# Kernel optimization log

Measured on AMD Instinct MI355X. Metric: run time of the kernel, lower is better.

## Reference

```python
import jax, jax.numpy as jnp
import numpy as np

N_NODES = 50000


def gcn_conv(x, row, col, deg_inv_sqrt, W, b, num_nodes):
    # PyG GCNConv: h = x @ W; out[i] = sum_{(j->i)} norm_ji * h[j] + b
    # norm_ji = deg^{-1/2}[j] * deg^{-1/2}[i], with self-loops already in (row, col).
    h = x @ W  # [N, C_out]
    norm = deg_inv_sqrt[row] * deg_inv_sqrt[col]  # [E+N]
    msgs = h[row] * norm[:, None]  # gather + scale, [E+N, C_out]
    out = jax.ops.segment_sum(msgs, col, num_segments=num_nodes)
    return out + b


def setup_inputs() -> dict:
    key = jax.random.key(0)
    ks = jax.random.split(key, 8)
    n, e = N_NODES, 1600000
    c_in, c_hid, c_out = 128, 64, 32
    x = jax.random.normal(ks[0], (n, c_in), dtype=jnp.float32)
    edge_index = jax.random.randint(ks[1], (2, e), 0, n, dtype=jnp.int64)
    s1 = 1.0 / np.sqrt(c_in)
    s2 = 1.0 / np.sqrt(c_hid)
    W1 = jax.random.uniform(ks[2], (c_in, c_hid), jnp.float32, -s1, s1)
    b1 = jnp.zeros((c_hid,), jnp.float32)
    W2 = jax.random.uniform(ks[3], (c_hid, c_out), jnp.float32, -s2, s2)
    b2 = jnp.zeros((c_out,), jnp.float32)
    W3 = jax.random.uniform(ks[4], (c_hid, c_out), jnp.float32, -s2, s2)
    b3 = jnp.zeros((c_out,), jnp.float32)
    return {"x": x, "edge_index": edge_index, "W1": W1, "b1": b1,
            "W2": W2, "b2": b2, "W3": W3, "b3": b3}


def reference(x, edge_index, W1, b1, W2, b2, W3, b3):
    n = x.shape[0]
    # add self-loops (PyG GCNConv default add_self_loops=True)
    loop = jnp.arange(n, dtype=edge_index.dtype)
    row = jnp.concatenate([edge_index[0], loop])
    col = jnp.concatenate([edge_index[1], loop])
    # symmetric normalization: deg computed over target nodes (unit edge weights)
    deg = jax.ops.segment_sum(jnp.ones_like(col, dtype=x.dtype), col, num_segments=n)
    deg_inv_sqrt = jnp.where(deg > 0, jax.lax.rsqrt(jnp.maximum(deg, 1.0)), 0.0)
    h = jax.nn.relu(gcn_conv(x, row, col, deg_inv_sqrt, W1, b1, n))
    mu = gcn_conv(h, row, col, deg_inv_sqrt, W2, b2, n)
    logvar = gcn_conv(h, row, col, deg_inv_sqrt, W3, b3, n)
    return (mu, logvar)
```

## Files before the change

### kernel.cpp

```cpp
#include <hip/hip_runtime.h>


#define NBMAX 256
#define NT2 256
#define SLOT 128
#define CAPSH 14
#define CAP (1 << CAPSH)

typedef unsigned int uint4v __attribute__((ext_vector_type(4)));
typedef float float4v __attribute__((ext_vector_type(4)));

__device__ __forceinline__ ushort f2bf(float x) {
    unsigned u = __float_as_uint(x);
    u = (u + 0x7FFFu + ((u >> 16) & 1u)) >> 16;
    return (ushort)u;
}
__device__ __forceinline__ float bflo(unsigned u) { return __uint_as_float(u << 16); }
__device__ __forceinline__ float bfhi(unsigned u) { return __uint_as_float(u & 0xFFFF0000u); }

__device__ __forceinline__ void acc8(float* a, uint4 x) {
    a[0] += bflo(x.x); a[1] += bfhi(x.x);
    a[2] += bflo(x.y); a[3] += bfhi(x.y);
    a[4] += bflo(x.z); a[5] += bfhi(x.z);
    a[6] += bflo(x.w); a[7] += bfhi(x.w);
}

__device__ __forceinline__ unsigned sc2(unsigned u, float d) {
    return (unsigned)f2bf(d * bflo(u)) | ((unsigned)f2bf(d * bfhi(u)) << 16);
}

__global__ __launch_bounds__(256) void k_front(const int* __restrict__ row,
                                               const int* __restrict__ col,
                                               const float* __restrict__ x,
                                               const float* __restrict__ W1,
                                               int* __restrict__ binbuf,
                                               unsigned char* __restrict__ cnt,
                                               ushort* __restrict__ hs1b,
                                               int n, int e, int chunk) {
    __shared__ __align__(16) unsigned char smem[16384];
    int t = threadIdx.x;
    if (blockIdx.x < NT2) {
        int* lh = (int*)smem;
        int tile = blockIdx.x;
        int t0 = tile * chunk;
        int t1 = t0 + chunk < e ? t0 + chunk : e;
        for (int i = t; i < NBMAX; i += 256) lh[i] = 0;
        __syncthreads();
        for (int i = t0 + t; i < t1; i += 256) {
            int c = col[i];
            int b = c >> 8;
            int pos = atomicAdd(&lh[b], 1);
            if (pos < SLOT)
                binbuf[(((b << 8) + tile) << 7) + pos] = row[i] | ((c & 255) << 16);
        }
        __syncthreads();
        for (int b = t; b < NBMAX; b += 256) {
            int c = lh[b];
            cnt[(tile << 8) + b] = (unsigned char)(c < SLOT ? c : SLOT);
        }
    } else {
        float4 (*ws)[64] = reinterpret_cast<float4(*)[64]>(smem);
        float4 (*xs)[16][8] = reinterpret_cast<float4(*)[16][8]>(smem + 8192);
        int wid = t >> 6;
        int lane = t & 63;
        int r0 = (blockIdx.x - NT2) * 64 + wid * 16;
        const float4* x4 = (const float4*)x;
        const float4* W4g = (const float4*)W1;
        float acc[16];
#pragma unroll
        for (int r = 0; r < 16; ++r) acc[r] = 0.f;
#pragma unroll
        for (int st = 0; st < 4; ++st) {
            if (st) __syncthreads();
#pragma unroll
            for (int j = 0; j < 2; ++j) {
                int f = j * 256 + t;
                float4 wv = W4g[st * 512 + f];
                int klocal = f >> 4;
                int c0 = (f & 15) * 4;
                int k4 = klocal >> 2, comp = klocal & 3;
                ((float*)&ws[k4][c0])[comp]     = wv.x;
                ((float*)&ws[k4][c0 + 1])[comp] = wv.y;
                ((float*)&ws[k4][c0 + 2])[comp] = wv.z;
                ((float*)&ws[k4][c0 + 3])[comp] = wv.w;
            }
#pragma unroll
            for (int j = 0; j < 2; ++j) {
                int idx = j * 64 + lane;
                int rr = r0 + (idx >> 3);
                if (rr >= n) rr = n - 1;
                xs[wid][idx >> 3][idx & 7] = x4[(size_t)rr * 32 + st * 8 + (idx & 7)];
            }
            __syncthreads();
#pragma unroll 2
            for (int k4 = 0; k4 < 8; ++k4) {
                float4 wv = ws[k4][lane];
#pragma unroll
                for (int r = 0; r < 16; ++r) {
                    float4 xv = xs[wid][r][k4];
                    acc[r] = fmaf(xv.x, wv.x, acc[r]);
                    acc[r] = fmaf(xv.y, wv.y, acc[r]);
                    acc[r] = fmaf(xv.z, wv.z, acc[r]);
                    acc[r] = fmaf(xv.w, wv.w, acc[r]);
                }
            }
        }
        ushort* hb = hs1b + (size_t)(lane >> 5) * n * 32 + (lane & 31);
#pragma unroll
        for (int r = 0; r < 16; ++r) {
            int rw = r0 + r;
            if (rw < n) hb[(size_t)rw * 32] = f2bf(acc[r]);
        }
    }
}

__global__ __launch_bounds__(256) void k_build(const int* __restrict__ binbuf,
                                               const unsigned char* __restrict__ cnt,
                                               float* __restrict__ dis,
                                               int* __restrict__ rp2,
                                               ushort* __restrict__ csr,
                                               ushort* __restrict__ hs1b, int n) {
    __shared__ int lcnt[256], s[256], cur[256];
    __shared__ float sdis[256];
    int b = blockIdx.x;
    int t = threadIdx.x;
    int myc = cnt[(t << 8) + b];
    int mybase = ((b << 8) + t) << 7;
    lcnt[t] = 0;
    __syncthreads();
    for (int i = 0; i < myc; ++i) {
        int p = binbuf[mybase + i];
        atomicAdd(&lcnt[(p >> 16) & 255], 1);
    }
    __syncthreads();
    int v = lcnt[t];
    s[t] = v;
    __syncthreads();
    for (int off = 1; off < 256; off <<= 1) {
        int u = (t >= off) ? s[t - off] : 0;
        __syncthreads();
        s[t] += u;
        __syncthreads();
    }
    int node0 = b << 8;
    int nloc = n - node0 < 256 ? n - node0 : 256;
    int lo = b << CAPSH;
    if (t < nloc) {
        int beg = lo + s[t] - v;
        rp2[2 * (node0 + t)] = beg;
        rp2[2 * (node0 + t) + 1] = beg + v;
        cur[t] = beg;
        float dv = rsqrtf((float)v + 1.0f);
        dis[node0 + t] = dv;
        sdis[t] = dv;
    }
    __syncthreads();
    for (int i = 0; i < myc; ++i) {
        int p = binbuf[mybase + i];
        int pos = atomicAdd(&cur[(p >> 16) & 255], 1);
        csr[pos] = (ushort)(p & 0xffff);
    }
    uint4* s0 = (uint4*)hs1b + (size_t)node0 * 4;
    uint4* s1 = (uint4*)hs1b + (size_t)n * 4 + (size_t)node0 * 4;
    for (int idx = t; idx < nloc * 4; idx += 256) {
        float dv = sdis[idx >> 2];
        uint4 u0 = s0[idx], u1 = s1[idx];
        u0.x = sc2(u0.x, dv); u0.y = sc2(u0.y, dv);
        u0.z = sc2(u0.z, dv); u0.w = sc2(u0.w, dv);
        u1.x = sc2(u1.x, dv); u1.y = sc2(u1.y, dv);
        u1.z = sc2(u1.z, dv); u1.w = sc2(u1.w, dv);
        s0[idx] = u0;
        s1[idx] = u1;
    }
}

__global__ __launch_bounds__(256) void k_pull1(const int* __restrict__ rp2,
                                               const ushort* __restrict__ csr,
                                               const ushort* __restrict__ hs1b,
                                               const float* __restrict__ dis,
                                               const float* __restrict__ b1,
                                               ushort* __restrict__ hs2b, int n) {
    int xcd = blockIdx.x & 7;
    int sid = xcd >> 2;
    int idx = (blockIdx.x >> 3) * 4 + (xcd & 3);
    int node = idx * 64 + (threadIdx.x >> 2);
    int c4 = threadIdx.x & 3;
    if (node >= n) return;
    size_t slab = (size_t)sid * n * 32;
    const uint4* h4 = (const uint4*)(hs1b + slab);
    int2 be = ((const int2*)rp2)[node];
    float a[8], b[8];
    uint4 v = h4[(size_t)node * 4 + c4];
    a[0] = bflo(v.x); a[1] = bfhi(v.x); a[2] = bflo(v.y); a[3] = bfhi(v.y);
    a[4] = bflo(v.z); a[5] = bfhi(v.z); a[6] = bflo(v.w); a[7] = bfhi(v.w);
#pragma unroll
    for (int j = 0; j < 8; ++j) b[j] = 0.f;
    int k = be.x;
    for (; k + 8 <= be.y; k += 8) {
        uint4 v0 = h4[(size_t)csr[k] * 4 + c4];
        uint4 v1 = h4[(size_t)csr[k + 1] * 4 + c4];
        uint4 v2 = h4[(size_t)csr[k + 2] * 4 + c4];
        uint4 v3 = h4[(size_t)csr[k + 3] * 4 + c4];
        uint4 v4 = h4[(size_t)csr[k + 4] * 4 + c4];
        uint4 v5 = h4[(size_t)csr[k + 5] * 4 + c4];
        uint4 v6 = h4[(size_t)csr[k + 6] * 4 + c4];
        uint4 v7 = h4[(size_t)csr[k + 7] * 4 + c4];
        acc8(a, v0); acc8(b, v1); acc8(a, v2); acc8(b, v3);
        acc8(a, v4); acc8(b, v5); acc8(a, v6); acc8(b, v7);
    }
    if (k + 4 <= be.y) {
        uint4 v0 = h4[(size_t)csr[k] * 4 + c4];
        uint4 v1 = h4[(size_t)csr[k + 1] * 4 + c4];
        uint4 v2 = h4[(size_t)csr[k + 2] * 4 + c4];
        uint4 v3 = h4[(size_t)csr[k + 3] * 4 + c4];
        acc8(a, v0); acc8(b, v1); acc8(a, v2); acc8(b, v3);
        k += 4;
    }
    for (; k < be.y; ++k) acc8(a, h4[(size_t)csr[k] * 4 + c4]);
    float d = dis[node];
    const float* b1s = b1 + sid * 32;
    float4 bb0 = *(const float4*)(b1s + c4 * 8);
    float4 bb1 = *(const float4*)(b1s + c4 * 8 + 4);
    float bj[8] = {bb0.x, bb0.y, bb0.z, bb0.w, bb1.x, bb1.y, bb1.z, bb1.w};
    float o[8];
#pragma unroll
    for (int j = 0; j < 8; ++j) {
        float tt = fmaf(d, a[j] + b[j], bj[j]);
        o[j] = tt > 0.f ? d * tt : 0.f;
    }
    uint4v w;
    w.x = (unsigned)f2bf(o[0]) | ((unsigned)f2bf(o[1]) << 16);
    w.y = (unsigned)f2bf(o[2]) | ((unsigned)f2bf(o[3]) << 16);
    w.z = (unsigned)f2bf(o[4]) | ((unsigned)f2bf(o[5]) << 16);
    w.w = (unsigned)f2bf(o[6]) | ((unsigned)f2bf(o[7]) << 16);
    __builtin_nontemporal_store(w, (uint4v*)((uint4*)(hs2b + slab) + (size_t)node * 4 + c4));
}

__global__ __launch_bounds__(256) void k_pull2(const int* __restrict__ rp2,
                                               const ushort* __restrict__ csr,
                                               const ushort* __restrict__ hs2b,
                                               const float* __restrict__ dis,
                                               float* __restrict__ gagg, int n) {
    int xcd = blockIdx.x & 7;
    int sid = xcd >> 2;
    int idx = (blockIdx.x >> 3) * 4 + (xcd & 3);
    int node = idx * 64 + (threadIdx.x >> 2);
    int c4 = threadIdx.x & 3;
    if (node >= n) return;
    const uint4* h4 = (const uint4*)(hs2b + (size_t)sid * n * 32);
    int2 be = ((const int2*)rp2)[node];
    float a[8], b[8];
    uint4 v = h4[(size_t)node * 4 + c4];
    a[0] = bflo(v.x); a[1] = bfhi(v.x); a[2] = bflo(v.y); a[3] = bfhi(v.y);
    a[4] = bflo(v.z); a[5] = bfhi(v.z); a[6] = bflo(v.w); a[7] = bfhi(v.w);
#pragma unroll
    for (int j = 0; j < 8; ++j) b[j] = 0.f;
    int k = be.x;
    for (; k + 8 <= be.y; k += 8) {
        uint4 v0 = h4[(size_t)csr[k] * 4 + c4];
        uint4 v1 = h4[(size_t)csr[k + 1] * 4 + c4];
        uint4 v2 = h4[(size_t)csr[k + 2] * 4 + c4];
        uint4 v3 = h4[(size_t)csr[k + 3] * 4 + c4];
        uint4 v4 = h4[(size_t)csr[k + 4] * 4 + c4];
        uint4 v5 = h4[(size_t)csr[k + 5] * 4 + c4];
        uint4 v6 = h4[(size_t)csr[k + 6] * 4 + c4];
        uint4 v7 = h4[(size_t)csr[k + 7] * 4 + c4];
        acc8(a, v0); acc8(b, v1); acc8(a, v2); acc8(b, v3);
        acc8(a, v4); acc8(b, v5); acc8(a, v6); acc8(b, v7);
    }
    if (k + 4 <= be.y) {
        uint4 v0 = h4[(size_t)csr[k] * 4 + c4];
        uint4 v1 = h4[(size_t)csr[k + 1] * 4 + c4];
        uint4 v2 = h4[(size_t)csr[k + 2] * 4 + c4];
        uint4 v3 = h4[(size_t)csr[k + 3] * 4 + c4];
        acc8(a, v0); acc8(b, v1); acc8(a, v2); acc8(b, v3);
        k += 4;
    }
    for (; k < be.y; ++k) acc8(a, h4[(size_t)csr[k] * 4 + c4]);
    float d = dis[node];
    float* dst = gagg + (size_t)node * 64 + sid * 32 + c4 * 8;
    float4v o0 = {d * (a[0] + b[0]), d * (a[1] + b[1]),
                  d * (a[2] + b[2]), d * (a[3] + b[3])};
    float4v o1 = {d * (a[4] + b[4]), d * (a[5] + b[5]),
                  d * (a[6] + b[6]), d * (a[7] + b[7])};
    __builtin_nontemporal_store(o0, (float4v*)dst);
    __builtin_nontemporal_store(o1, (float4v*)(dst + 4));
}

__global__ __launch_bounds__(256) void k_gemm23(const float* __restrict__ g,
                                                const float* __restrict__ W2,
                                                const float* __restrict__ b2,
                                                const float* __restrict__ W3,
                                                const float* __restrict__ b3,
                                                float* __restrict__ out, int n) {
    __shared__ float ws[2 * 32 * 17 * 4];
    __shared__ float4 gs[4][16 * 16];
    for (int i = threadIdx.x; i < 64 * 32; i += 256) {
        int k = i >> 5, c = i & 31;
        int a = (c * 17 + (k >> 2)) * 4 + (k & 3);
        ws[a] = W2[i];
        ws[2176 + a] = W3[i];
    }
    int wid = threadIdx.x >> 6;
    int lane = threadIdx.x & 63;
    int half = lane >> 5;
    int ch = lane & 31;
    int r0 = blockIdx.x * 64 + wid * 16;
    const float4* g4 = (const float4*)g;
#pragma unroll
    for (int j = 0; j < 4; ++j) {
        int idx = j * 64 + lane;
        int rr = r0 + (idx >> 4);
        if (rr >= n) rr = n - 1;
        gs[wid][idx] = g4[(size_t)rr * 16 + (idx & 15)];
    }
    __syncthreads();
    float acc[16];
#pragma unroll
    for (int r = 0; r < 16; ++r) acc[r] = 0.f;
    const float4* wl = (const float4*)ws;
    const float4* gw = gs[wid];
#pragma unroll 2
    for (int k4 = 0; k4 < 16; ++k4) {
        float4 wv = wl[half * 544 + ch * 17 + k4];
#pragma unroll
        for (int r = 0; r < 16; ++r) {
            float4 gv = gw[r * 16 + k4];
            acc[r] = fmaf(gv.x, wv.x, acc[r]);
            acc[r] = fmaf(gv.y, wv.y, acc[r]);
            acc[r] = fmaf(gv.z, wv.z, acc[r]);
            acc[r] = fmaf(gv.w, wv.w, acc[r]);
        }
    }
    float bb = half ? b3[ch] : b2[ch];
    size_t obase = half ? (size_t)n * 32 : 0;
#pragma unroll
    for (int r = 0; r < 16; ++r) {
        int rw = r0 + r;
        if (rw < n)
            __builtin_nontemporal_store(acc[r] + bb, out + obase + (size_t)rw * 32 + ch);
    }
}

extern "C" void kernel_launch(void* const* d_in, const int* in_sizes, int n_in,
                              void* d_out, int out_size, void* d_ws, size_t ws_size,
                              hipStream_t stream) {
    const float* x  = (const float*)d_in[0];
    const int*   ei = (const int*)d_in[1];
    const float* W1 = (const float*)d_in[2];
    const float* b1 = (const float*)d_in[3];
    const float* W2 = (const float*)d_in[4];
    const float* b2 = (const float*)d_in[5];
    const float* W3 = (const float*)d_in[6];
    const float* b3 = (const float*)d_in[7];

    int n = in_sizes[0] / 128;
    int e = in_sizes[1] / 2;
    int nb = (n + 255) >> 8;
    const int* row = ei;
    const int* col = ei + e;

    float* fws   = (float*)d_ws;
    float* dis   = fws;
    ushort* hs1b = (ushort*)(fws + n);
    ushort* hs2b = hs1b + (size_t)2 * n * 32;
    int* rp2     = (int*)(hs2b + (size_t)2 * n * 32);
    ushort* csr  = (ushort*)(rp2 + 2 * (size_t)n);
    float* gagg  = (float*)(csr + (size_t)nb * CAP);
    int* binbuf  = (int*)(gagg + (size_t)n * 64);
    unsigned char* cnt = (unsigned char*)(binbuf + (size_t)nb * NT2 * SLOT);
    float* out   = (float*)d_out;

    int chunk = (e + NT2 - 1) / NT2;
    int ntiles = (n + 63) / 64;
    int pg = ntiles;
    int pgrid = 8 * ((pg + 3) / 4);

    dim3 blk(256);
    k_front<<<NT2 + ntiles, blk, 0, stream>>>(row, col, x, W1, binbuf, cnt, hs1b, n, e, chunk);
    k_build<<<nb, blk, 0, stream>>>(binbuf, cnt, dis, rp2, csr, hs1b, n);
    k_pull1<<<pgrid, blk, 0, stream>>>(rp2, csr, hs1b, dis, b1, hs2b, n);
    k_pull2<<<pgrid, blk, 0, stream>>>(rp2, csr, hs2b, dis, gagg, n);
    k_gemm23<<<(n + 63) / 64, blk, 0, stream>>>(gagg, W2, b2, W3, b3, out, n);
}
```

Before: 118.3 us.

## Process two nodes per thread in pull kernels and store layer-2 aggregate as bf16

Each thread in both pull kernels now aggregates two adjacent nodes, interleaving their neighbor gathers so more independent loads are in flight, and reads both row ranges with a single int4 load. The intermediate aggregate passed to the final GEMM is written as bf16 instead of fp32, halving its write and read traffic, and the GEMM widens it back to fp32 in shared memory. This costs extra rounding precision and adds imbalance when the two nodes' degrees differ, since the shared loop runs only while both have four or more edges left.

```diff
diff --git a/kernel.cpp b/kernel.cpp
--- a/kernel.cpp
+++ b/kernel.cpp
@@ -8,7 +8,6 @@
 #define CAP (1 << CAPSH)
 
 typedef unsigned int uint4v __attribute__((ext_vector_type(4)));
-typedef float float4v __attribute__((ext_vector_type(4)));
 
 __device__ __forceinline__ ushort f2bf(float x) {
     unsigned u = __float_as_uint(x);
@@ -23,6 +22,13 @@
     a[2] += bflo(x.y); a[3] += bfhi(x.y);
     a[4] += bflo(x.z); a[5] += bfhi(x.z);
     a[6] += bflo(x.w); a[7] += bfhi(x.w);
+}
+
+__device__ __forceinline__ void self8(float* a, uint4 x) {
+    a[0] = bflo(x.x); a[1] = bfhi(x.x);
+    a[2] = bflo(x.y); a[3] = bfhi(x.y);
+    a[4] = bflo(x.z); a[5] = bfhi(x.z);
+    a[6] = bflo(x.w); a[7] = bfhi(x.w);
 }
 
 __device__ __forceinline__ unsigned sc2(unsigned u, float d) {
@@ -183,111 +189,158 @@
     int xcd = blockIdx.x & 7;
     int sid = xcd >> 2;
     int idx = (blockIdx.x >> 3) * 4 + (xcd & 3);
-    int node = idx * 64 + (threadIdx.x >> 2);
+    int n0 = idx * 128 + (threadIdx.x >> 2) * 2;
     int c4 = threadIdx.x & 3;
-    if (node >= n) return;
+    if (n0 >= n) return;
+    bool has1 = n0 + 1 < n;
     size_t slab = (size_t)sid * n * 32;
     const uint4* h4 = (const uint4*)(hs1b + slab);
-    int2 be = ((const int2*)rp2)[node];
-    float a[8], b[8];
-    uint4 v = h4[(size_t)node * 4 + c4];
-    a[0] = bflo(v.x); a[1] = bfhi(v.x); a[2] = bflo(v.y); a[3] = bfhi(v.y);
-    a[4] = bflo(v.z); a[5] = bfhi(v.z); a[6] = bflo(v.w); a[7] = bfhi(v.w);
-#pragma unroll
-    for (int j = 0; j < 8; ++j) b[j] = 0.f;
-    int k = be.x;
-    for (; k + 8 <= be.y; k += 8) {
-        uint4 v0 = h4[(size_t)csr[k] * 4 + c4];
-        uint4 v1 = h4[(size_t)csr[k + 1] * 4 + c4];
-        uint4 v2 = h4[(size_t)csr[k + 2] * 4 + c4];
-        uint4 v3 = h4[(size_t)csr[k + 3] * 4 + c4];
-        uint4 v4 = h4[(size_t)csr[k + 4] * 4 + c4];
-        uint4 v5 = h4[(size_t)csr[k + 5] * 4 + c4];
-        uint4 v6 = h4[(size_t)csr[k + 6] * 4 + c4];
-        uint4 v7 = h4[(size_t)csr[k + 7] * 4 + c4];
-        acc8(a, v0); acc8(b, v1); acc8(a, v2); acc8(b, v3);
-        acc8(a, v4); acc8(b, v5); acc8(a, v6); acc8(b, v7);
-    }
-    if (k + 4 <= be.y) {
-        uint4 v0 = h4[(size_t)csr[k] * 4 + c4];
-        uint4 v1 = h4[(size_t)csr[k + 1] * 4 + c4];
-        uint4 v2 = h4[(size_t)csr[k + 2] * 4 + c4];
-        uint4 v3 = h4[(size_t)csr[k + 3] * 4 + c4];
-        acc8(a, v0); acc8(b, v1); acc8(a, v2); acc8(b, v3);
-        k += 4;
-    }
-    for (; k < be.y; ++k) acc8(a, h4[(size_t)csr[k] * 4 + c4]);
-    float d = dis[node];
+    int4 be = ((const int4*)rp2)[n0 >> 1];
+    float a0[8], a1[8];
+    self8(a0, h4[(size_t)n0 * 4 + c4]);
+    if (has1) self8(a1, h4[(size_t)(n0 + 1) * 4 + c4]);
+    else { be.z = 0; be.w = 0;
+#pragma unroll
+        for (int j = 0; j < 8; ++j) a1[j] = 0.f; }
+    int k0 = be.x, k1 = be.z;
+    while (k0 + 4 <= be.y && k1 + 4 <= be.w) {
+        uint4 v0 = h4[(size_t)csr[k0] * 4 + c4];
+        uint4 v1 = h4[(size_t)csr[k0 + 1] * 4 + c4];
+        uint4 v2 = h4[(size_t)csr[k0 + 2] * 4 + c4];
+        uint4 v3 = h4[(size_t)csr[k0 + 3] * 4 + c4];
+        uint4 w0 = h4[(size_t)csr[k1] * 4 + c4];
+        uint4 w1 = h4[(size_t)csr[k1 + 1] * 4 + c4];
+        uint4 w2 = h4[(size_t)csr[k1 + 2] * 4 + c4];
+        uint4 w3 = h4[(size_t)csr[k1 + 3] * 4 + c4];
+        acc8(a0, v0); acc8(a1, w0); acc8(a0, v1); acc8(a1, w1);
+        acc8(a0, v2); acc8(a1, w2); acc8(a0, v3); acc8(a1, w3);
+        k0 += 4; k1 += 4;
+    }
+    for (; k0 + 4 <= be.y; k0 += 4) {
+        uint4 v0 = h4[(size_t)csr[k0] * 4 + c4];
+        uint4 v1 = h4[(size_t)csr[k0 + 1] * 4 + c4];
+        uint4 v2 = h4[(size_t)csr[k0 + 2] * 4 + c4];
+        uint4 v3 = h4[(size_t)csr[k0 + 3] * 4 + c4];
+        acc8(a0, v0); acc8(a0, v1); acc8(a0, v2); acc8(a0, v3);
+    }
+    for (; k1 + 4 <= be.w; k1 += 4) {
+        uint4 w0 = h4[(size_t)csr[k1] * 4 + c4];
+        uint4 w1 = h4[(size_t)csr[k1 + 1] * 4 + c4];
+        uint4 w2 = h4[(size_t)csr[k1 + 2] * 4 + c4];
+        uint4 w3 = h4[(size_t)csr[k1 + 3] * 4 + c4];
+        acc8(a1, w0); acc8(a1, w1); acc8(a1, w2); acc8(a1, w3);
+    }
+    for (; k0 < be.y; ++k0) acc8(a0, h4[(size_t)csr[k0] * 4 + c4]);
+    for (; k1 < be.w; ++k1) acc8(a1, h4[(size_t)csr[k1] * 4 + c4]);
     const float* b1s = b1 + sid * 32;
     float4 bb0 = *(const float4*)(b1s + c4 * 8);
     float4 bb1 = *(const float4*)(b1s + c4 * 8 + 4);
     float bj[8] = {bb0.x, bb0.y, bb0.z, bb0.w, bb1.x, bb1.y, bb1.z, bb1.w};
-    float o[8];
-#pragma unroll
-    for (int j = 0; j < 8; ++j) {
-        float tt = fmaf(d, a[j] + b[j], bj[j]);
-        o[j] = tt > 0.f ? d * tt : 0.f;
-    }
-    uint4v w;
-    w.x = (unsigned)f2bf(o[0]) | ((unsigned)f2bf(o[1]) << 16);
-    w.y = (unsigned)f2bf(o[2]) | ((unsigned)f2bf(o[3]) << 16);
-    w.z = (unsigned)f2bf(o[4]) | ((unsigned)f2bf(o[5]) << 16);
-    w.w = (unsigned)f2bf(o[6]) | ((unsigned)f2bf(o[7]) << 16);
-    __builtin_nontemporal_store(w, (uint4v*)((uint4*)(hs2b + slab) + (size_t)node * 4 + c4));
+    uint4* outp = (uint4*)(hs2b + slab);
+    {
+        float d = dis[n0];
+        float o[8];
+#pragma unroll
+        for (int j = 0; j < 8; ++j) {
+            float tt = fmaf(d, a0[j], bj[j]);
+            o[j] = tt > 0.f ? d * tt : 0.f;
+        }
+        uint4v w;
+        w.x = (unsigned)f2bf(o[0]) | ((unsigned)f2bf(o[1]) << 16);
+        w.y = (unsigned)f2bf(o[2]) | ((unsigned)f2bf(o[3]) << 16);
+        w.z = (unsigned)f2bf(o[4]) | ((unsigned)f2bf(o[5]) << 16);
+        w.w = (unsigned)f2bf(o[6]) | ((unsigned)f2bf(o[7]) << 16);
+        __builtin_nontemporal_store(w, (uint4v*)(outp + (size_t)n0 * 4 + c4));
+    }
+    if (has1) {
+        float d = dis[n0 + 1];
+        float o[8];
+#pragma unroll
+        for (int j = 0; j < 8; ++j) {
+            float tt = fmaf(d, a1[j], bj[j]);
+            o[j] = tt > 0.f ? d * tt : 0.f;
+        }
+        uint4v w;
+        w.x = (unsigned)f2bf(o[0]) | ((unsigned)f2bf(o[1]) << 16);
+        w.y = (unsigned)f2bf(o[2]) | ((unsigned)f2bf(o[3]) << 16);
+        w.z = (unsigned)f2bf(o[4]) | ((unsigned)f2bf(o[5]) << 16);
+        w.w = (unsigned)f2bf(o[6]) | ((unsigned)f2bf(o[7]) << 16);
+        __builtin_nontemporal_store(w, (uint4v*)(outp + (size_t)(n0 + 1) * 4 + c4));
+    }
 }
 
 __global__ __launch_bounds__(256) void k_pull2(const int* __restrict__ rp2,
                                                const ushort* __restrict__ csr,
                                                const ushort* __restrict__ hs2b,
                                                const float* __restrict__ dis,
-                                               float* __restrict__ gagg, int n) {
+                                               ushort* __restrict__ gaggb, int n) {
     int xcd = blockIdx.x & 7;
     int sid = xcd >> 2;
     int idx = (blockIdx.x >> 3) * 4 + (xcd & 3);
-    int node = idx * 64 + (threadIdx.x >> 2);
+    int n0 = idx * 128 + (threadIdx.x >> 2) * 2;
     int c4 = threadIdx.x & 3;
-    if (node >= n) return;
+    if (n0 >= n) return;
+    bool has1 = n0 + 1 < n;
     const uint4* h4 = (const uint4*)(hs2b + (size_t)sid * n * 32);
-    int2 be = ((const int2*)rp2)[node];
-    float a[8], b[8];
-    uint4 v = h4[(size_t)node * 4 + c4];
-    a[0] = bflo(v.x); a[1] = bfhi(v.x); a[2] = bflo(v.y); a[3] = bfhi(v.y);
-    a[4] = bflo(v.z); a[5] = bfhi(v.z); a[6] = bflo(v.w); a[7] = bfhi(v.w);
-#pragma unroll
-    for (int j = 0; j < 8; ++j) b[j] = 0.f;
-    int k = be.x;
-    for (; k + 8 <= be.y; k += 8) {
-        uint4 v0 = h4[(size_t)csr[k] * 4 + c4];
-        uint4 v1 = h4[(size_t)csr[k + 1] * 4 + c4];
-        uint4 v2 = h4[(size_t)csr[k + 2] * 4 + c4];
-        uint4 v3 = h4[(size_t)csr[k + 3] * 4 + c4];
-        uint4 v4 = h4[(size_t)csr[k + 4] * 4 + c4];
-        uint4 v5 = h4[(size_t)csr[k + 5] * 4 + c4];
-        uint4 v6 = h4[(size_t)csr[k + 6] * 4 + c4];
-        uint4 v7 = h4[(size_t)csr[k + 7] * 4 + c4];
-        acc8(a, v0); acc8(b, v1); acc8(a, v2); acc8(b, v3);
-        acc8(a, v4); acc8(b, v5); acc8(a, v6); acc8(b, v7);
-    }
-    if (k + 4 <= be.y) {
-        uint4 v0 = h4[(size_t)csr[k] * 4 + c4];
-        uint4 v1 = h4[(size_t)csr[k + 1] * 4 + c4];
-        uint4 v2 = h4[(size_t)csr[k + 2] * 4 + c4];
-        uint4 v3 = h4[(size_t)csr[k + 3] * 4 + c4];
-        acc8(a, v0); acc8(b, v1); acc8(a, v2); acc8(b, v3);
-        k += 4;
-    }
-    for (; k < be.y; ++k) acc8(a, h4[(size_t)csr[k] * 4 + c4]);
-    float d = dis[node];
-    float* dst = gagg + (size_t)node * 64 + sid * 32 + c4 * 8;
-    float4v o0 = {d * (a[0] + b[0]), d * (a[1] + b[1]),
-                  d * (a[2] + b[2]), d * (a[3] + b[3])};
-    float4v o1 = {d * (a[4] + b[4]), d * (a[5] + b[5]),
-                  d * (a[6] + b[6]), d * (a[7] + b[7])};
-    __builtin_nontemporal_store(o0, (float4v*)dst);
-    __builtin_nontemporal_store(o1, (float4v*)(dst + 4));
-}
-
-__global__ __launch_bounds__(256) void k_gemm23(const float* __restrict__ g,
+    int4 be = ((const int4*)rp2)[n0 >> 1];
+    float a0[8], a1[8];
+    self8(a0, h4[(size_t)n0 * 4 + c4]);
+    if (has1) self8(a1, h4[(size_t)(n0 + 1) * 4 + c4]);
+    else { be.z = 0; be.w = 0;
+#pragma unroll
+        for (int j = 0; j < 8; ++j) a1[j] = 0.f; }
+    int k0 = be.x, k1 = be.z;
+    while (k0 + 4 <= be.y && k1 + 4 <= be.w) {
+        uint4 v0 = h4[(size_t)csr[k0] * 4 + c4];
+        uint4 v1 = h4[(size_t)csr[k0 + 1] * 4 + c4];
+        uint4 v2 = h4[(size_t)csr[k0 + 2] * 4 + c4];
+        uint4 v3 = h4[(size_t)csr[k0 + 3] * 4 + c4];
+        uint4 w0 = h4[(size_t)csr[k1] * 4 + c4];
+        uint4 w1 = h4[(size_t)csr[k1 + 1] * 4 + c4];
+        uint4 w2 = h4[(size_t)csr[k1 + 2] * 4 + c4];
+        uint4 w3 = h4[(size_t)csr[k1 + 3] * 4 + c4];
+        acc8(a0, v0); acc8(a1, w0); acc8(a0, v1); acc8(a1, w1);
+        acc8(a0, v2); acc8(a1, w2); acc8(a0, v3); acc8(a1, w3);
+        k0 += 4; k1 += 4;
+    }
+    for (; k0 + 4 <= be.y; k0 += 4) {
+        uint4 v0 = h4[(size_t)csr[k0] * 4 + c4];
+        uint4 v1 = h4[(size_t)csr[k0 + 1] * 4 + c4];
+        uint4 v2 = h4[(size_t)csr[k0 + 2] * 4 + c4];
+        uint4 v3 = h4[(size_t)csr[k0 + 3] * 4 + c4];
+        acc8(a0, v0); acc8(a0, v1); acc8(a0, v2); acc8(a0, v3);
+    }
+    for (; k1 + 4 <= be.w; k1 += 4) {
+        uint4 w0 = h4[(size_t)csr[k1] * 4 + c4];
+        uint4 w1 = h4[(size_t)csr[k1 + 1] * 4 + c4];
+        uint4 w2 = h4[(size_t)csr[k1 + 2] * 4 + c4];
+        uint4 w3 = h4[(size_t)csr[k1 + 3] * 4 + c4];
+        acc8(a1, w0); acc8(a1, w1); acc8(a1, w2); acc8(a1, w3);
+    }
+    for (; k0 < be.y; ++k0) acc8(a0, h4[(size_t)csr[k0] * 4 + c4]);
+    for (; k1 < be.w; ++k1) acc8(a1, h4[(size_t)csr[k1] * 4 + c4]);
+    uint4* outp = (uint4*)gaggb;
+    {
+        float d = dis[n0];
+        uint4v w;
+        w.x = (unsigned)f2bf(d * a0[0]) | ((unsigned)f2bf(d * a0[1]) << 16);
+        w.y = (unsigned)f2bf(d * a0[2]) | ((unsigned)f2bf(d * a0[3]) << 16);
+        w.z = (unsigned)f2bf(d * a0[4]) | ((unsigned)f2bf(d * a0[5]) << 16);
+        w.w = (unsigned)f2bf(d * a0[6]) | ((unsigned)f2bf(d * a0[7]) << 16);
+        __builtin_nontemporal_store(w, (uint4v*)(outp + (size_t)n0 * 8 + sid * 4 + c4));
+    }
+    if (has1) {
+        float d = dis[n0 + 1];
+        uint4v w;
+        w.x = (unsigned)f2bf(d * a1[0]) | ((unsigned)f2bf(d * a1[1]) << 16);
+        w.y = (unsigned)f2bf(d * a1[2]) | ((unsigned)f2bf(d * a1[3]) << 16);
+        w.z = (unsigned)f2bf(d * a1[4]) | ((unsigned)f2bf(d * a1[5]) << 16);
+        w.w = (unsigned)f2bf(d * a1[6]) | ((unsigned)f2bf(d * a1[7]) << 16);
+        __builtin_nontemporal_store(w, (uint4v*)(outp + (size_t)(n0 + 1) * 8 + sid * 4 + c4));
+    }
+}
+
+__global__ __launch_bounds__(256) void k_gemm23(const ushort* __restrict__ gaggb,
                                                 const float* __restrict__ W2,
                                                 const float* __restrict__ b2,
                                                 const float* __restrict__ W3,
@@ -306,13 +359,16 @@
     int half = lane >> 5;
     int ch = lane & 31;
     int r0 = blockIdx.x * 64 + wid * 16;
-    const float4* g4 = (const float4*)g;
-#pragma unroll
-    for (int j = 0; j < 4; ++j) {
+    const uint4* g4 = (const uint4*)gaggb;
+#pragma unroll
+    for (int j = 0; j < 2; ++j) {
         int idx = j * 64 + lane;
-        int rr = r0 + (idx >> 4);
+        int rr = r0 + (idx >> 3);
         if (rr >= n) rr = n - 1;
-        gs[wid][idx] = g4[(size_t)rr * 16 + (idx & 15)];
+        uint4 u = g4[(size_t)rr * 8 + (idx & 7)];
+        int base = (idx >> 3) * 16 + (idx & 7) * 2;
+        gs[wid][base]     = make_float4(bflo(u.x), bfhi(u.x), bflo(u.y), bfhi(u.y));
+        gs[wid][base + 1] = make_float4(bflo(u.z), bfhi(u.z), bflo(u.w), bfhi(u.w));
     }
     __syncthreads();
     float acc[16];
@@ -366,20 +422,20 @@
     ushort* hs2b = hs1b + (size_t)2 * n * 32;
     int* rp2     = (int*)(hs2b + (size_t)2 * n * 32);
     ushort* csr  = (ushort*)(rp2 + 2 * (size_t)n);
-    float* gagg  = (float*)(csr + (size_t)nb * CAP);
-    int* binbuf  = (int*)(gagg + (size_t)n * 64);
+    ushort* gaggb = csr + (size_t)nb * CAP;
+    int* binbuf  = (int*)(gaggb + (size_t)n * 64);
     unsigned char* cnt = (unsigned char*)(binbuf + (size_t)nb * NT2 * SLOT);
     float* out   = (float*)d_out;
 
     int chunk = (e + NT2 - 1) / NT2;
     int ntiles = (n + 63) / 64;
-    int pg = ntiles;
-    int pgrid = 8 * ((pg + 3) / 4);
+    int pnb = (n + 127) / 128;
+    int pgrid = 8 * ((pnb + 3) / 4);
 
     dim3 blk(256);
     k_front<<<NT2 + ntiles, blk, 0, stream>>>(row, col, x, W1, binbuf, cnt, hs1b, n, e, chunk);
     k_build<<<nb, blk, 0, stream>>>(binbuf, cnt, dis, rp2, csr, hs1b, n);
     k_pull1<<<pgrid, blk, 0, stream>>>(rp2, csr, hs1b, dis, b1, hs2b, n);
-    k_pull2<<<pgrid, blk, 0, stream>>>(rp2, csr, hs2b, dis, gagg, n);
-    k_gemm23<<<(n + 63) / 64, blk, 0, stream>>>(gagg, W2, b2, W3, b3, out, n);
-}
+    k_pull2<<<pgrid, blk, 0, stream>>>(rp2, csr, hs2b, dis, gaggb, n);
+    k_gemm23<<<(n + 63) / 64, blk, 0, stream>>>(gaggb, W2, b2, W3, b3, out, n);
+}
```

After: 135.4 us. 1.15x slower.
